# Optimization experiments

Measured on AMD Instinct MI355X. Metric: run time of the kernel, lower is better.

The kernel has to match this reference:

```python
import jax, jax.numpy as jnp
import numpy as np
from jax import lax

EPS = 1e-5

def _bn(x, p):
    # p: [4, C] = (gamma, beta, running_mean, running_var); x: [B,C,H,W] (eval-mode BN)
    g, b, m, v = p
    return (x - m[None, :, None, None]) * (g / jnp.sqrt(v + EPS))[None, :, None, None] + b[None, :, None, None]

def _relu6(x):
    return jnp.clip(x, 0.0, 6.0)

def _grouped_1x1(x, w):
    # x: [B, D, H, W], w: [G, D//G]; groups=G, 1 out channel per group (contiguous channel groups)
    B, D, H, W = x.shape
    G = w.shape[0]
    xr = x.reshape(B, G, D // G, H, W)
    return jnp.einsum('bgihw,gi->bghw', xr, w)

def _pool4(x, kind):
    if kind == 'max':
        return lax.reduce_window(x, -jnp.inf, lax.max, (1, 1, 4, 4), (1, 1, 4, 4), 'VALID')
    s = lax.reduce_window(x, 0.0, lax.add, (1, 1, 4, 4), (1, 1, 4, 4), 'VALID')
    return s / 16.0

def _rel_pos_index(rh):
    # Swin-style relative position index, static numpy
    coords = np.stack(np.meshgrid(np.arange(rh), np.arange(rh), indexing='ij')).reshape(2, -1)
    rel = coords[:, :, None] - coords[:, None, :]
    rel = rel.transpose(1, 2, 0).astype(np.int64)
    rel[..., 0] += rh - 1
    rel[..., 1] += rh - 1
    rel[..., 0] *= 2 * rh - 1
    return rel.sum(-1)  # [N, N]

def _upsample_bilinear_align(x, scale):
    # UpsamplingBilinear2d => align_corners=True
    B, C, H, W = x.shape
    Ho, Wo = H * scale, W * scale
    ys = jnp.linspace(0.0, H - 1.0, Ho)
    xs = jnp.linspace(0.0, W - 1.0, Wo)
    y0 = jnp.floor(ys).astype(jnp.int32); y1 = jnp.minimum(y0 + 1, H - 1); wy = (ys - y0)[None, None, :, None]
    x0 = jnp.floor(xs).astype(jnp.int32); x1 = jnp.minimum(x0 + 1, W - 1); wx = (xs - x0)[None, None, None, :]
    rows = x[:, :, y0, :] * (1.0 - wy) + x[:, :, y1, :] * wy          # [B,C,Ho,W]
    return rows[:, :, :, x0] * (1.0 - wx) + rows[:, :, :, x1] * wx    # [B,C,Ho,Wo]

def bh_attention(x, w_le, b_le, bn_le, w_max, b_max, bn_max, w_avg, b_avg, bn_avg,
                 bias_table, w_q, w_kv, w_proj, b_proj, w_out, b_out):
    D = x.shape[1]
    G = D // 4
    # q branch: 4x4 stride-4 grouped conv (groups=G, 4 in-ch per group) + BN + ReLU6
    xq = lax.conv_general_dilated(x, w_le, window_strides=(4, 4), padding='VALID',
                                  dimension_numbers=('NCHW', 'OIHW', 'NCHW'),
                                  feature_group_count=G)
    xq = _relu6(_bn(xq + b_le[None, :, None, None], bn_le))
    B, C, H, W = xq.shape
    N = H * W
    nH = 4 if C > 64 else 2
    hd = C // nH
    xq_t = xq.reshape(B, C, N).transpose(0, 2, 1)                      # [B,N,C]
    q = (xq_t @ w_q).reshape(B, N, nH, hd).transpose(0, 2, 1, 3) * (hd ** -0.5)

    def kv_branch(t, w_g, b_g, bn_g):
        t = _relu6(_bn(_grouped_1x1(t, w_g) + b_g[None, :, None, None], bn_g))
        tt = t.reshape(B, C, N).transpose(0, 2, 1)                     # [B,N,C]
        kv = (tt @ w_kv).reshape(B, N, 2, nH, hd).transpose(2, 0, 3, 1, 4)
        return kv[0], kv[1]                                            # [B,nH,N,hd]

    k1, v1 = kv_branch(_pool4(x, 'max'), w_max, b_max, bn_max)
    k2, v2 = kv_branch(_pool4(x, 'avg'), w_avg, b_avg, bn_avg)

    idx = _rel_pos_index(H)
    bias = bias_table[idx.reshape(-1)].reshape(N, N, nH).transpose(2, 0, 1)[None]  # [1,nH,N,N]

    def attend(k, v):
        attn = jax.nn.softmax(jnp.einsum('bhnd,bhmd->bhnm', q, k) + bias, axis=-1)
        o = jnp.einsum('bhnm,bhmd->bhnd', attn, v).transpose(0, 2, 1, 3).reshape(B, N, C)
        return o @ w_proj + b_proj

    x1 = attend(k1, v1).reshape(B, H, W, C).transpose(0, 3, 1, 2)
    x2 = attend(k2, v2).reshape(B, H, W, C).transpose(0, 3, 1, 2)
    out = x1 + x2
    out = jnp.einsum('bchw,oc->bohw', out, w_out) + b_out[None, :, None, None]
    return _upsample_bilinear_align(out, 4)


def setup_inputs() -> dict:
    key = jax.random.key(0)
    dim, h, B = 384, 128, 8
    C = dim // 4            # 96
    nH = 4 if C > 64 else 2
    rh = h // 4             # 32
    ks = jax.random.split(key, 12)
    bn_id = jnp.stack([jnp.ones(C), jnp.zeros(C), jnp.zeros(C), jnp.ones(C)])
    inp = {
        'x': jax.random.normal(ks[0], (B, dim, h, h), jnp.float32),
        'w_le': jax.random.normal(ks[1], (C, 4, 4, 4), jnp.float32) * 0.05,
        'b_le': jnp.zeros((C,), jnp.float32),
        'bn_le': bn_id,
        'w_max': jax.random.normal(ks[2], (C, 4), jnp.float32) * 0.1,
        'b_max': jnp.zeros((C,), jnp.float32),
        'bn_max': bn_id,
        'w_avg': jax.random.normal(ks[3], (C, 4), jnp.float32) * 0.1,
        'b_avg': jnp.zeros((C,), jnp.float32),
        'bn_avg': bn_id,
        'bias_table': jax.random.normal(ks[4], ((2 * rh - 1) ** 2, nH), jnp.float32) * 0.02,
        'w_q': jax.random.normal(ks[5], (C, C), jnp.float32) * (C ** -0.5),
        'w_kv': jax.random.normal(ks[6], (C, 2 * C), jnp.float32) * (C ** -0.5),
        'w_proj': jax.random.normal(ks[7], (C, C), jnp.float32) * (C ** -0.5),
        'b_proj': jnp.zeros((C,), jnp.float32),
        'w_out': jax.random.normal(ks[8], (dim, C), jnp.float32) * (C ** -0.5),
        'b_out': jnp.zeros((dim,), jnp.float32),
    }
    return inp


def reference(x, w_le, b_le, bn_le, w_max, b_max, bn_max, w_avg, b_avg, bn_avg,
              bias_table, w_q, w_kv, w_proj, b_proj, w_out, b_out):
    return bh_attention(x, w_le, b_le, bn_le, w_max, b_max, bn_max, w_avg, b_avg, bn_avg,
                        bias_table, w_q, w_kv, w_proj, b_proj, w_out, b_out)
```

## Files before the change

### kernel.cpp

```cpp
#include <hip/hip_runtime.h>
#include <math.h>

namespace {
constexpr int Bb  = 8;
constexpr int Dd  = 384;
constexpr int HIN = 128;
constexpr int Cc  = 96;
constexpr int Nn  = 1024;
constexpr int NH  = 4;
constexpr int HD  = 24;
}
#define BN_EPS 1e-5f
#define QSCALE 0.20412414523193154f

typedef unsigned short u16;
typedef unsigned int   u32;
typedef __attribute__((ext_vector_type(8))) short bh8;
typedef __attribute__((ext_vector_type(4))) float fx4;

#define MFMA16(a,b,c) __builtin_amdgcn_mfma_f32_16x16x32_bf16((a),(b),(c),0,0,0)

union PackU { u32 u[4]; bh8 s; };

__device__ __forceinline__ void split1(float v, u16& hi, u16& lo) {
    const u32 bv = __float_as_uint(v);
    const u32 hb = bv & 0xffff0000u;
    hi = (u16)(bv >> 16);
    const float r = v - __uint_as_float(hb);
    lo = (u16)(__float_as_uint(r) >> 16);
}
__device__ __forceinline__ void split2(float x, float y, u32& hi, u32& lo) {
    const u32 bx = __float_as_uint(x), by = __float_as_uint(y);
    const u32 hx = bx & 0xffff0000u, hy = by & 0xffff0000u;
    hi = (hx >> 16) | hy;
    const float rx = x - __uint_as_float(hx);
    const float ry = y - __uint_as_float(hy);
    lo = (__float_as_uint(rx) >> 16) | (__float_as_uint(ry) & 0xffff0000u);
}

__device__ __forceinline__ float bn_relu6(float y, const float* __restrict__ bn, int c) {
    float gam = bn[c], bet = bn[Cc + c], mu = bn[2*Cc + c], var = bn[3*Cc + c];
    float s = gam / sqrtf(var + BN_EPS);
    float r = (y - mu) * s + bet;
    return fminf(fmaxf(r, 0.0f), 6.0f);
}

__global__ __launch_bounds__(256) void stem_kernel(
    const float* __restrict__ x, const float* __restrict__ w_le,
    const float* __restrict__ b_le, const float* __restrict__ bn_le,
    const float* __restrict__ w_max, const float* __restrict__ b_max, const float* __restrict__ bn_max,
    const float* __restrict__ w_avg, const float* __restrict__ b_avg, const float* __restrict__ bn_avg,
    float* __restrict__ xq, float* __restrict__ tmx, float* __restrict__ tav)
{
    const int tid = threadIdx.x;
    const int n = blockIdx.x * 256 + tid;
    const int g = blockIdx.y;
    const int b = blockIdx.z;
    const int oh = n >> 5, ow = n & 31;

    const float* xb = x + (((size_t)b * Dd + 4*g) * HIN + 4*oh) * HIN + 4*ow;
    float conv = 0.0f, mxv = 0.0f, avv = 0.0f;
    #pragma unroll
    for (int i = 0; i < 4; ++i) {
        float cmax = -3.0e38f, csum = 0.0f;
        #pragma unroll
        for (int kh = 0; kh < 4; ++kh) {
            const float4 v = *(const float4*)(xb + ((size_t)i * HIN + kh) * HIN);
            const float* wl = w_le + (((g*4 + i)*4 + kh) * 4);
            conv = fmaf(v.x, wl[0], conv);
            conv = fmaf(v.y, wl[1], conv);
            conv = fmaf(v.z, wl[2], conv);
            conv = fmaf(v.w, wl[3], conv);
            cmax = fmaxf(cmax, fmaxf(fmaxf(v.x, v.y), fmaxf(v.z, v.w)));
            csum += (v.x + v.y) + (v.z + v.w);
        }
        mxv = fmaf(cmax, w_max[g*4 + i], mxv);
        avv = fmaf(csum * (1.0f/16.0f), w_avg[g*4 + i], avv);
    }
    const float xqv = bn_relu6(conv + b_le[g], bn_le, g);
    const float tm  = bn_relu6(mxv  + b_max[g], bn_max, g);
    const float ta  = bn_relu6(avv  + b_avg[g], bn_avg, g);
    const size_t o = ((size_t)b * Cc + g) * Nn + n;
    xq[o] = xqv; tmx[o] = tm; tav[o] = ta;
}

__global__ __launch_bounds__(256) void proj_kernel(
    const float* __restrict__ xq, const float* __restrict__ tmx, const float* __restrict__ tav,
    const float* __restrict__ w_q, const float* __restrict__ w_kv,
    u16* __restrict__ qhp, u16* __restrict__ qlp,
    u16* __restrict__ k1h, u16* __restrict__ k1l, u16* __restrict__ k2h, u16* __restrict__ k2l,
    u16* __restrict__ v1h, u16* __restrict__ v1l, u16* __restrict__ v2h, u16* __restrict__ v2l)
{
    const int tid = threadIdx.x;
    const int n0 = blockIdx.x * 32;
    const int b  = blockIdx.y;
    __shared__ float axq[32*101];
    __shared__ float amx[32*101];
    __shared__ float aav[32*101];
    __shared__ float lw[96*97];

    for (int e = tid; e < 96*32; e += 256) {
        const int c = e >> 5, j = e & 31;
        const size_t src = ((size_t)b * Cc + c) * Nn + n0 + j;
        axq[j*101 + c] = xq[src];
        amx[j*101 + c] = tmx[src];
        aav[j*101 + c] = tav[src];
    }

    const int tn = (tid & 7) * 4;
    const int tc = (tid >> 3) * 3;

    __syncthreads();
    for (int e = tid; e < 96*96; e += 256) lw[(e/96)*97 + (e%96)] = w_q[e];
    __syncthreads();
    {
        float acc[4][3] = {};
        for (int k = 0; k < 96; ++k) {
            const float w0 = lw[k*97 + tc + 0];
            const float w1 = lw[k*97 + tc + 1];
            const float w2 = lw[k*97 + tc + 2];
            #pragma unroll
            for (int i = 0; i < 4; ++i) {
                const float a = axq[(tn+i)*101 + k];
                acc[i][0] = fmaf(a, w0, acc[i][0]);
                acc[i][1] = fmaf(a, w1, acc[i][1]);
                acc[i][2] = fmaf(a, w2, acc[i][2]);
            }
        }
        #pragma unroll
        for (int j = 0; j < 3; ++j) {
            const int col = tc + j, hh = col / HD, d = col - hh*HD;
            #pragma unroll
            for (int i = 0; i < 4; ++i) {
                const int n = n0 + tn + i;
                u16 hi, lo;
                split1(acc[i][j] * QSCALE, hi, lo);
                const size_t dst = ((size_t)(b*NH + hh)*Nn + n)*32 + d;
                qhp[dst] = hi; qlp[dst] = lo;
            }
        }
    }

    __syncthreads();
    for (int e = tid; e < 96*96; e += 256) lw[(e/96)*97 + (e%96)] = w_kv[(e/96)*192 + (e%96)];
    __syncthreads();
    {
        float a1c[4][3] = {}, a2c[4][3] = {};
        for (int k = 0; k < 96; ++k) {
            const float w0 = lw[k*97 + tc + 0];
            const float w1 = lw[k*97 + tc + 1];
            const float w2 = lw[k*97 + tc + 2];
            #pragma unroll
            for (int i = 0; i < 4; ++i) {
                const float a1 = amx[(tn+i)*101 + k];
                const float a2 = aav[(tn+i)*101 + k];
                a1c[i][0] = fmaf(a1, w0, a1c[i][0]);
                a1c[i][1] = fmaf(a1, w1, a1c[i][1]);
                a1c[i][2] = fmaf(a1, w2, a1c[i][2]);
                a2c[i][0] = fmaf(a2, w0, a2c[i][0]);
                a2c[i][1] = fmaf(a2, w1, a2c[i][1]);
                a2c[i][2] = fmaf(a2, w2, a2c[i][2]);
            }
        }
        #pragma unroll
        for (int j = 0; j < 3; ++j) {
            const int col = tc + j, hh = col / HD, d = col - hh*HD;
            #pragma unroll
            for (int i = 0; i < 4; ++i) {
                const int n = n0 + tn + i;
                const int rho = (n & ~31) | ((n & 4) << 2) | ((n & 24) >> 1) | (n & 3);
                const size_t dst = ((size_t)(b*NH + hh)*Nn + rho)*32 + d;
                u16 hi, lo;
                split1(a1c[i][j], hi, lo); k1h[dst] = hi; k1l[dst] = lo;
                split1(a2c[i][j], hi, lo); k2h[dst] = hi; k2l[dst] = lo;
            }
        }
    }

    __syncthreads();
    for (int e = tid; e < 96*96; e += 256) lw[(e/96)*97 + (e%96)] = w_kv[(e/96)*192 + 96 + (e%96)];
    __syncthreads();
    {
        float a1c[4][3] = {}, a2c[4][3] = {};
        for (int k = 0; k < 96; ++k) {
            const float w0 = lw[k*97 + tc + 0];
            const float w1 = lw[k*97 + tc + 1];
            const float w2 = lw[k*97 + tc + 2];
            #pragma unroll
            for (int i = 0; i < 4; ++i) {
                const float a1 = amx[(tn+i)*101 + k];
                const float a2 = aav[(tn+i)*101 + k];
                a1c[i][0] = fmaf(a1, w0, a1c[i][0]);
                a1c[i][1] = fmaf(a1, w1, a1c[i][1]);
                a1c[i][2] = fmaf(a1, w2, a1c[i][2]);
                a2c[i][0] = fmaf(a2, w0, a2c[i][0]);
                a2c[i][1] = fmaf(a2, w1, a2c[i][1]);
                a2c[i][2] = fmaf(a2, w2, a2c[i][2]);
            }
        }
        #pragma unroll
        for (int j = 0; j < 3; ++j) {
            const int col = tc + j, hh = col / HD, d = col - hh*HD;
            #pragma unroll
            for (int i = 0; i < 4; ++i) {
                const int n = n0 + tn + i;
                const size_t dst = ((size_t)(b*NH + hh)*32 + d)*Nn + n;
                u16 hi, lo;
                split1(a1c[i][j], hi, lo); v1h[dst] = hi; v1l[dst] = lo;
                split1(a2c[i][j], hi, lo); v2h[dst] = hi; v2l[dst] = lo;
            }
        }
    }

    for (int e = tid; e < 1024; e += 256) {
        const int hh = e >> 8;
        const int nn = (e >> 3) & 31;
        const int d  = 24 + (e & 7);
        const int n  = n0 + nn;
        const size_t kd = ((size_t)(b*NH + hh)*Nn + n)*32 + d;
        qhp[kd] = 0; qlp[kd] = 0;
        k1h[kd] = 0; k1l[kd] = 0; k2h[kd] = 0; k2l[kd] = 0;
        const size_t vd = ((size_t)(b*NH + hh)*32 + d)*Nn + n;
        v1h[vd] = 0; v1l[vd] = 0; v2h[vd] = 0; v2l[vd] = 0;
    }
}

__global__ __launch_bounds__(256) void attn_kernel(
    const u16* __restrict__ qhp, const u16* __restrict__ qlp,
    const u16* __restrict__ k1h, const u16* __restrict__ k1l,
    const u16* __restrict__ k2h, const u16* __restrict__ k2l,
    const u16* __restrict__ v1h, const u16* __restrict__ v1l,
    const u16* __restrict__ v2h, const u16* __restrict__ v2l,
    const float* __restrict__ bias_table, float* __restrict__ osum)
{
    const int tid = threadIdx.x;
    const int h = blockIdx.y, b = blockIdx.z;
    const int bh = b*NH + h;

    __shared__ float biasl[3969];
    for (int e = tid; e < 3969; e += 256) biasl[e] = bias_table[e*NH + h];
    __syncthreads();

    const int lane = tid & 63;
    const int wave = tid >> 6;
    const int lg = lane >> 4;
    const int lr = lane & 15;
    const int q  = blockIdx.x*64 + wave*16 + lr;
    const int yn = q >> 5, xn = q & 31;

    const size_t qoff = ((size_t)bh*Nn + q)*32 + lg*8;
    const bh8 qfh = *(const bh8*)(qhp + qoff);
    const bh8 qfl = *(const bh8*)(qlp + qoff);

    const size_t kbase = ((size_t)bh*Nn + lr)*32 + lg*8;
    const u16* kp1h = k1h + kbase;
    const u16* kp1l = k1l + kbase;
    const u16* kp2h = k2h + kbase;
    const u16* kp2l = k2l + kbase;
    const size_t vbase = ((size_t)bh*32 + lr)*Nn + lg*8;
    const u16* vp1h = v1h + vbase;
    const u16* vp1l = v1l + vbase;
    const u16* vp2h = v2h + vbase;
    const u16* vp2l = v2l + vbase;

    const fx4 zero = {0.0f, 0.0f, 0.0f, 0.0f};
    fx4 o1[2], o2[2];
    o1[0] = zero; o1[1] = zero; o2[0] = zero; o2[1] = zero;
    float m1 = -3.0e38f, m2 = -3.0e38f, l1 = 0.0f, l2 = 0.0f;

    for (int it = 0; it < 16; ++it) {
        const int kb = it*64;
        fx4 s1[4], s2[4];
        #pragma unroll
        for (int t = 0; t < 4; ++t) {
            const int ro = (kb + t*16)*32;
            const bh8 a1h = *(const bh8*)(kp1h + ro);
            const bh8 a1l = *(const bh8*)(kp1l + ro);
            const bh8 a2h = *(const bh8*)(kp2h + ro);
            const bh8 a2l = *(const bh8*)(kp2l + ro);
            const int ym   = (kb >> 5) + (t >> 1);
            const int xmb  = (t & 1)*4 + lg*8;
            const int rowb = (yn - ym + 31)*63 + (xn + 31) - xmb;
            fx4 cb;
            #pragma unroll
            for (int j = 0; j < 4; ++j) cb[j] = biasl[rowb - j];
            fx4 u1 = cb, u2 = cb;
            u1 = MFMA16(a1h, qfh, u1);
            u1 = MFMA16(a1h, qfl, u1);
            u1 = MFMA16(a1l, qfh, u1);
            u2 = MFMA16(a2h, qfh, u2);
            u2 = MFMA16(a2h, qfl, u2);
            u2 = MFMA16(a2l, qfh, u2);
            s1[t] = u1; s2[t] = u2;
        }

        float t1 = s1[0][0], t2 = s2[0][0];
        #pragma unroll
        for (int t = 0; t < 4; ++t)
            #pragma unroll
            for (int j = 0; j < 4; ++j) {
                if (t | j) { t1 = fmaxf(t1, s1[t][j]); t2 = fmaxf(t2, s2[t][j]); }
            }
        t1 = fmaxf(t1, __shfl_xor(t1, 16));
        t1 = fmaxf(t1, __shfl_xor(t1, 32));
        t2 = fmaxf(t2, __shfl_xor(t2, 16));
        t2 = fmaxf(t2, __shfl_xor(t2, 32));
        const float M1 = fmaxf(m1, t1), M2 = fmaxf(m2, t2);
        const float c1 = __expf(m1 - M1), c2 = __expf(m2 - M2);
        m1 = M1; m2 = M2;
        l1 *= c1; l2 *= c2;
        o1[0] *= c1; o1[1] *= c1;
        o2[0] *= c2; o2[1] *= c2;

        float p1[4][4], p2[4][4];
        #pragma unroll
        for (int t = 0; t < 4; ++t)
            #pragma unroll
            for (int j = 0; j < 4; ++j) {
                const float e1 = __expf(s1[t][j] - M1);
                const float e2 = __expf(s2[t][j] - M2);
                p1[t][j] = e1; p2[t][j] = e2;
                l1 += e1; l2 += e2;
            }

        #pragma unroll
        for (int ch = 0; ch < 2; ++ch) {
            PackU b1h, b1l, b2h, b2l;
            split2(p1[2*ch  ][0], p1[2*ch  ][1], b1h.u[0], b1l.u[0]);
            split2(p1[2*ch  ][2], p1[2*ch  ][3], b1h.u[1], b1l.u[1]);
            split2(p1[2*ch+1][0], p1[2*ch+1][1], b1h.u[2], b1l.u[2]);
            split2(p1[2*ch+1][2], p1[2*ch+1][3], b1h.u[3], b1l.u[3]);
            split2(p2[2*ch  ][0], p2[2*ch  ][1], b2h.u[0], b2l.u[0]);
            split2(p2[2*ch  ][2], p2[2*ch  ][3], b2h.u[1], b2l.u[1]);
            split2(p2[2*ch+1][0], p2[2*ch+1][1], b2h.u[2], b2l.u[2]);
            split2(p2[2*ch+1][2], p2[2*ch+1][3], b2h.u[3], b2l.u[3]);
            const int vo0 = kb + ch*32;
            #pragma unroll
            for (int dt = 0; dt < 2; ++dt) {
                const size_t vo = (size_t)(dt*16)*Nn + vo0;
                const bh8 w1h = *(const bh8*)(vp1h + vo);
                const bh8 w1l = *(const bh8*)(vp1l + vo);
                const bh8 w2h = *(const bh8*)(vp2h + vo);
                const bh8 w2l = *(const bh8*)(vp2l + vo);
                o1[dt] = MFMA16(w1h, b1h.s, o1[dt]);
                o1[dt] = MFMA16(w1h, b1l.s, o1[dt]);
                o1[dt] = MFMA16(w1l, b1h.s, o1[dt]);
                o2[dt] = MFMA16(w2h, b2h.s, o2[dt]);
                o2[dt] = MFMA16(w2h, b2l.s, o2[dt]);
                o2[dt] = MFMA16(w2l, b2h.s, o2[dt]);
            }
        }
    }

    l1 += __shfl_xor(l1, 16); l1 += __shfl_xor(l1, 32);
    l2 += __shfl_xor(l2, 16); l2 += __shfl_xor(l2, 32);
    const float i1 = 1.0f / l1, i2 = 1.0f / l2;
    float* orow = osum + ((size_t)b*Nn + q)*Cc + h*HD;
    #pragma unroll
    for (int dt = 0; dt < 2; ++dt)
        #pragma unroll
        for (int j = 0; j < 4; ++j) {
            const int d = dt*16 + lg*4 + j;
            if (d < HD) orow[d] = o1[dt][j]*i1 + o2[dt][j]*i2;
        }
}

__global__ __launch_bounds__(256) void fusew_kernel(
    const float* __restrict__ w_proj, const float* __restrict__ b_proj,
    const float* __restrict__ w_out, const float* __restrict__ b_out,
    float* __restrict__ wf, float* __restrict__ bf)
{
    const int e = blockIdx.x * 256 + threadIdx.x;
    if (e < Cc * Dd) {
        const int c = e / Dd, o = e - c*Dd;
        const float* wp = w_proj + c*Cc;
        const float* wo = w_out + (size_t)o*Cc;
        float acc = 0.0f;
        for (int c2 = 0; c2 < Cc; ++c2) acc = fmaf(wp[c2], wo[c2], acc);
        wf[e] = acc;
    }
    if (e < Dd) {
        const float* wo = w_out + (size_t)e*Cc;
        float acc = 0.0f;
        for (int c = 0; c < Cc; ++c) acc = fmaf(b_proj[c], wo[c], acc);
        bf[e] = b_out[e] + 2.0f * acc;
    }
}

__global__ __launch_bounds__(256) void outgemm_kernel(
    const float* __restrict__ osum, const float* __restrict__ wf, const float* __restrict__ bf,
    float* __restrict__ outs)
{
    const int tid = threadIdx.x;
    const int n0 = blockIdx.x * 32;
    const int b  = blockIdx.y;
    __shared__ float ax[32*101];
    __shared__ float lw[96*132];
    for (int e = tid; e < 32*96; e += 256) {
        const int n = e / 96, c = e - n*96;
        ax[n*101 + c] = osum[((size_t)b*Nn + n0 + n)*Cc + c];
    }
    const int tn = (tid & 7) * 4;
    const int tj = (tid >> 3) * 4;
    for (int o0 = 0; o0 < Dd; o0 += 128) {
        __syncthreads();
        for (int e = tid; e < 96*128; e += 256) {
            const int c = e >> 7, j = e & 127;
            lw[c*132 + j] = wf[(size_t)c*Dd + o0 + j];
        }
        __syncthreads();
        float acc[4][4] = {};
        for (int c = 0; c < 96; ++c) {
            const float4 wv = *(const float4*)&lw[c*132 + tj];
            #pragma unroll
            for (int i = 0; i < 4; ++i) {
                const float a = ax[(tn+i)*101 + c];
                acc[i][0] = fmaf(a, wv.x, acc[i][0]);
                acc[i][1] = fmaf(a, wv.y, acc[i][1]);
                acc[i][2] = fmaf(a, wv.z, acc[i][2]);
                acc[i][3] = fmaf(a, wv.w, acc[i][3]);
            }
        }
        #pragma unroll
        for (int j = 0; j < 4; ++j) {
            const int o = o0 + tj + j;
            const float bb = bf[o];
            #pragma unroll
            for (int i = 0; i < 4; ++i)
                outs[((size_t)b*Dd + o)*Nn + n0 + tn + i] = acc[i][j] + bb;
        }
    }
}

__global__ __launch_bounds__(256) void upsample_kernel(
    const float* __restrict__ src, float* __restrict__ dst)
{
    const int gid = blockIdx.x * 256 + threadIdx.x;
    const int ox4 = gid & 31;
    const int oy  = (gid >> 5) & 127;
    const int bc  = gid >> 12;
    const float* s = src + (size_t)bc * 1024;
    const float sy = oy * (31.0f / 127.0f);
    const int y0 = (int)sy;
    const int y1 = min(y0 + 1, 31);
    const float wy = sy - (float)y0;
    const float* r0 = s + y0 * 32;
    const float* r1 = s + y1 * 32;
    float res[4];
    #pragma unroll
    for (int j = 0; j < 4; ++j) {
        const int ox = ox4 * 4 + j;
        const float sx = ox * (31.0f / 127.0f);
        const int x0 = (int)sx;
        const int x1 = min(x0 + 1, 31);
        const float wx = sx - (float)x0;
        const float t0 = r0[x0] * (1.0f - wx) + r0[x1] * wx;
        const float t1 = r1[x0] * (1.0f - wx) + r1[x1] * wx;
        res[j] = t0 * (1.0f - wy) + t1 * wy;
    }
    *(float4*)(dst + (size_t)gid * 4) = make_float4(res[0], res[1], res[2], res[3]);
}

extern "C" void kernel_launch(void* const* d_in, const int* in_sizes, int n_in,
                              void* d_out, int out_size, void* d_ws, size_t ws_size,
                              hipStream_t stream)
{
    const float* x      = (const float*)d_in[0];
    const float* w_le   = (const float*)d_in[1];
    const float* b_le   = (const float*)d_in[2];
    const float* bn_le  = (const float*)d_in[3];
    const float* w_max  = (const float*)d_in[4];
    const float* b_max  = (const float*)d_in[5];
    const float* bn_max = (const float*)d_in[6];
    const float* w_avg  = (const float*)d_in[7];
    const float* b_avg  = (const float*)d_in[8];
    const float* bn_avg = (const float*)d_in[9];
    const float* btab   = (const float*)d_in[10];
    const float* w_q    = (const float*)d_in[11];
    const float* w_kv   = (const float*)d_in[12];
    const float* w_proj = (const float*)d_in[13];
    const float* b_proj = (const float*)d_in[14];
    const float* w_out  = (const float*)d_in[15];
    const float* b_out  = (const float*)d_in[16];
    (void)in_sizes; (void)n_in; (void)out_size; (void)ws_size;

    float* ws = (float*)d_ws;
    const size_t T  = (size_t)Bb * Cc * Nn;
    const size_t AS = (size_t)Bb * NH * Nn * 32;

    float* xq   = ws + 0*T;
    float* tmx  = ws + 1*T;
    float* tav  = ws + 2*T;
    u16*  bb16  = (u16*)(ws + 3*T);
    u16* qh  = bb16 + 0*AS;  u16* ql  = bb16 + 1*AS;
    u16* k1h = bb16 + 2*AS;  u16* k1l = bb16 + 3*AS;
    u16* k2h = bb16 + 4*AS;  u16* k2l = bb16 + 5*AS;
    u16* v1h = bb16 + 6*AS;  u16* v1l = bb16 + 7*AS;
    u16* v2h = bb16 + 8*AS;  u16* v2l = bb16 + 9*AS;
    float* osum = (float*)(bb16 + 10*AS);
    float* wf   = osum + T;
    float* bf   = wf + (size_t)Cc*Dd;
    float* outs = ws;

    stem_kernel<<<dim3(4, 96, 8), 256, 0, stream>>>(
        x, w_le, b_le, bn_le, w_max, b_max, bn_max, w_avg, b_avg, bn_avg, xq, tmx, tav);
    proj_kernel<<<dim3(32, 8), 256, 0, stream>>>(
        xq, tmx, tav, w_q, w_kv, qh, ql, k1h, k1l, k2h, k2l, v1h, v1l, v2h, v2l);
    fusew_kernel<<<dim3(144), 256, 0, stream>>>(w_proj, b_proj, w_out, b_out, wf, bf);
    attn_kernel<<<dim3(16, 4, 8), 256, 0, stream>>>(
        qh, ql, k1h, k1l, k2h, k2l, v1h, v1l, v2h, v2l, btab, osum);
    outgemm_kernel<<<dim3(32, 8), 256, 0, stream>>>(osum, wf, bf, outs);
    upsample_kernel<<<dim3(49152), 256, 0, stream>>>(outs, (float*)d_out);
}
```

Measured before the change: 545.8 us.

## Split attention keys across waves with flash-decoding merge and serialize branches

The attention kernel now handles 32 queries per block instead of 64 and splits the 1024 keys between two wave pairs. Each pair runs its own online softmax, and the partial max, sum and output are merged through shared memory. The two softmax branches are processed one after the other rather than interleaved, which lowers register pressure, and a launch bound of 4 blocks per CU is set. The rescale is skipped when the running max does not change. Together these double the grid and raise occupancy on a kernel that was latency bound, at the cost of one barrier, a shared-memory merge step and the bias table being loaded twice as often.

```diff
diff --git a/kernel.cpp b/kernel.cpp
--- a/kernel.cpp
+++ b/kernel.cpp
@@ -225,7 +225,7 @@
     }
 }
 
-__global__ __launch_bounds__(256) void attn_kernel(
+__global__ __launch_bounds__(256, 4) void attn_kernel(
     const u16* __restrict__ qhp, const u16* __restrict__ qlp,
     const u16* __restrict__ k1h, const u16* __restrict__ k1l,
     const u16* __restrict__ k2h, const u16* __restrict__ k2l,
@@ -238,14 +238,18 @@
     const int bh = b*NH + h;
 
     __shared__ float biasl[3969];
+    __shared__ float mrg[2][64][21];
+
     for (int e = tid; e < 3969; e += 256) biasl[e] = bias_table[e*NH + h];
     __syncthreads();
 
     const int lane = tid & 63;
     const int wave = tid >> 6;
+    const int qg = wave & 1;
+    const int ks = wave >> 1;
     const int lg = lane >> 4;
     const int lr = lane & 15;
-    const int q  = blockIdx.x*64 + wave*16 + lr;
+    const int q  = blockIdx.x*32 + qg*16 + lr;
     const int yn = q >> 5, xn = q & 31;
 
     const size_t qoff = ((size_t)bh*Nn + q)*32 + lg*8;
@@ -253,116 +257,133 @@
     const bh8 qfl = *(const bh8*)(qlp + qoff);
 
     const size_t kbase = ((size_t)bh*Nn + lr)*32 + lg*8;
-    const u16* kp1h = k1h + kbase;
-    const u16* kp1l = k1l + kbase;
-    const u16* kp2h = k2h + kbase;
-    const u16* kp2l = k2l + kbase;
     const size_t vbase = ((size_t)bh*32 + lr)*Nn + lg*8;
-    const u16* vp1h = v1h + vbase;
-    const u16* vp1l = v1l + vbase;
-    const u16* vp2h = v2h + vbase;
-    const u16* vp2l = v2l + vbase;
+    const u16* kph[2] = { k1h + kbase, k2h + kbase };
+    const u16* kpl[2] = { k1l + kbase, k2l + kbase };
+    const u16* vph[2] = { v1h + vbase, v2h + vbase };
+    const u16* vpl[2] = { v1l + vbase, v2l + vbase };
 
     const fx4 zero = {0.0f, 0.0f, 0.0f, 0.0f};
-    fx4 o1[2], o2[2];
-    o1[0] = zero; o1[1] = zero; o2[0] = zero; o2[1] = zero;
-    float m1 = -3.0e38f, m2 = -3.0e38f, l1 = 0.0f, l2 = 0.0f;
-
-    for (int it = 0; it < 16; ++it) {
-        const int kb = it*64;
-        fx4 s1[4], s2[4];
-        #pragma unroll
-        for (int t = 0; t < 4; ++t) {
-            const int ro = (kb + t*16)*32;
-            const bh8 a1h = *(const bh8*)(kp1h + ro);
-            const bh8 a1l = *(const bh8*)(kp1l + ro);
-            const bh8 a2h = *(const bh8*)(kp2h + ro);
-            const bh8 a2l = *(const bh8*)(kp2l + ro);
-            const int ym   = (kb >> 5) + (t >> 1);
-            const int xmb  = (t & 1)*4 + lg*8;
-            const int rowb = (yn - ym + 31)*63 + (xn + 31) - xmb;
-            fx4 cb;
-            #pragma unroll
-            for (int j = 0; j < 4; ++j) cb[j] = biasl[rowb - j];
-            fx4 u1 = cb, u2 = cb;
-            u1 = MFMA16(a1h, qfh, u1);
-            u1 = MFMA16(a1h, qfl, u1);
-            u1 = MFMA16(a1l, qfh, u1);
-            u2 = MFMA16(a2h, qfh, u2);
-            u2 = MFMA16(a2h, qfl, u2);
-            u2 = MFMA16(a2l, qfh, u2);
-            s1[t] = u1; s2[t] = u2;
-        }
-
-        float t1 = s1[0][0], t2 = s2[0][0];
-        #pragma unroll
-        for (int t = 0; t < 4; ++t)
+    fx4 oo[2][2];
+    float mm[2], ll[2];
+
+    #pragma unroll
+    for (int br = 0; br < 2; ++br) {
+        oo[br][0] = zero; oo[br][1] = zero;
+        float m = -3.0e38f, l = 0.0f;
+        const u16* kh = kph[br]; const u16* kl = kpl[br];
+        const u16* vh = vph[br]; const u16* vl = vpl[br];
+
+        for (int it = ks*8; it < ks*8 + 8; ++it) {
+            const int kb = it*64;
+            fx4 s[4];
+            #pragma unroll
+            for (int t = 0; t < 4; ++t) {
+                const int ro = (kb + t*16)*32;
+                const bh8 ah = *(const bh8*)(kh + ro);
+                const bh8 al = *(const bh8*)(kl + ro);
+                const int ym   = (kb >> 5) + (t >> 1);
+                const int xmb  = (t & 1)*4 + lg*8;
+                const int rowb = (yn - ym + 31)*63 + (xn + 31) - xmb;
+                fx4 u;
+                #pragma unroll
+                for (int j = 0; j < 4; ++j) u[j] = biasl[rowb - j];
+                u = MFMA16(ah, qfh, u);
+                u = MFMA16(ah, qfl, u);
+                u = MFMA16(al, qfh, u);
+                s[t] = u;
+            }
+
+            float tmax = s[0][0];
+            #pragma unroll
+            for (int t = 0; t < 4; ++t)
+                #pragma unroll
+                for (int j = 0; j < 4; ++j)
+                    if (t | j) tmax = fmaxf(tmax, s[t][j]);
+            tmax = fmaxf(tmax, __shfl_xor(tmax, 16));
+            tmax = fmaxf(tmax, __shfl_xor(tmax, 32));
+            const float M = fmaxf(m, tmax);
+            if (!__all(tmax <= m)) {
+                const float c = __expf(m - M);
+                l *= c;
+                oo[br][0] *= c; oo[br][1] *= c;
+            }
+            m = M;
+
+            #pragma unroll
+            for (int ch = 0; ch < 2; ++ch) {
+                const float e0 = __expf(s[2*ch  ][0] - M);
+                const float e1 = __expf(s[2*ch  ][1] - M);
+                const float e2 = __expf(s[2*ch  ][2] - M);
+                const float e3 = __expf(s[2*ch  ][3] - M);
+                const float e4 = __expf(s[2*ch+1][0] - M);
+                const float e5 = __expf(s[2*ch+1][1] - M);
+                const float e6 = __expf(s[2*ch+1][2] - M);
+                const float e7 = __expf(s[2*ch+1][3] - M);
+                l += ((e0 + e1) + (e2 + e3)) + ((e4 + e5) + (e6 + e7));
+                PackU ph_, pl_;
+                split2(e0, e1, ph_.u[0], pl_.u[0]);
+                split2(e2, e3, ph_.u[1], pl_.u[1]);
+                split2(e4, e5, ph_.u[2], pl_.u[2]);
+                split2(e6, e7, ph_.u[3], pl_.u[3]);
+                const int vo0 = kb + ch*32;
+                #pragma unroll
+                for (int dt = 0; dt < 2; ++dt) {
+                    const size_t vo = (size_t)(dt*16)*Nn + vo0;
+                    const bh8 wh = *(const bh8*)(vh + vo);
+                    const bh8 wl = *(const bh8*)(vl + vo);
+                    oo[br][dt] = MFMA16(wh, ph_.s, oo[br][dt]);
+                    oo[br][dt] = MFMA16(wh, pl_.s, oo[br][dt]);
+                    oo[br][dt] = MFMA16(wl, ph_.s, oo[br][dt]);
+                }
+            }
+        }
+        mm[br] = m; ll[br] = l;
+    }
+
+    if (ks == 1) {
+        float* mb = &mrg[qg][lane][0];
+        #pragma unroll
+        for (int br = 0; br < 2; ++br) {
+            mb[br*10 + 0] = mm[br];
+            mb[br*10 + 1] = ll[br];
             #pragma unroll
             for (int j = 0; j < 4; ++j) {
-                if (t | j) { t1 = fmaxf(t1, s1[t][j]); t2 = fmaxf(t2, s2[t][j]); }
-            }
-        t1 = fmaxf(t1, __shfl_xor(t1, 16));
-        t1 = fmaxf(t1, __shfl_xor(t1, 32));
-        t2 = fmaxf(t2, __shfl_xor(t2, 16));
-        t2 = fmaxf(t2, __shfl_xor(t2, 32));
-        const float M1 = fmaxf(m1, t1), M2 = fmaxf(m2, t2);
-        const float c1 = __expf(m1 - M1), c2 = __expf(m2 - M2);
-        m1 = M1; m2 = M2;
-        l1 *= c1; l2 *= c2;
-        o1[0] *= c1; o1[1] *= c1;
-        o2[0] *= c2; o2[1] *= c2;
-
-        float p1[4][4], p2[4][4];
-        #pragma unroll
-        for (int t = 0; t < 4; ++t)
+                mb[br*10 + 2 + j] = oo[br][0][j];
+                mb[br*10 + 6 + j] = oo[br][1][j];
+            }
+        }
+    }
+    __syncthreads();
+    if (ks == 0) {
+        const float* mb = &mrg[qg][lane][0];
+        float li[2]; fx4 om[2][2];
+        #pragma unroll
+        for (int br = 0; br < 2; ++br) {
+            const float mo  = mb[br*10 + 0];
+            const float lo2 = mb[br*10 + 1];
+            const float M  = fmaxf(mm[br], mo);
+            const float ca = __expf(mm[br] - M);
+            const float cb = __expf(mo - M);
+            float lm = ll[br]*ca + lo2*cb;
+            #pragma unroll
+            for (int dt = 0; dt < 2; ++dt)
+                #pragma unroll
+                for (int j = 0; j < 4; ++j)
+                    om[br][dt][j] = oo[br][dt][j]*ca + mb[br*10 + 2 + dt*4 + j]*cb;
+            lm += __shfl_xor(lm, 16);
+            lm += __shfl_xor(lm, 32);
+            li[br] = 1.0f / lm;
+        }
+        float* orow = osum + ((size_t)b*Nn + q)*Cc + h*HD;
+        #pragma unroll
+        for (int dt = 0; dt < 2; ++dt)
             #pragma unroll
             for (int j = 0; j < 4; ++j) {
-                const float e1 = __expf(s1[t][j] - M1);
-                const float e2 = __expf(s2[t][j] - M2);
-                p1[t][j] = e1; p2[t][j] = e2;
-                l1 += e1; l2 += e2;
-            }
-
-        #pragma unroll
-        for (int ch = 0; ch < 2; ++ch) {
-            PackU b1h, b1l, b2h, b2l;
-            split2(p1[2*ch  ][0], p1[2*ch  ][1], b1h.u[0], b1l.u[0]);
-            split2(p1[2*ch  ][2], p1[2*ch  ][3], b1h.u[1], b1l.u[1]);
-            split2(p1[2*ch+1][0], p1[2*ch+1][1], b1h.u[2], b1l.u[2]);
-            split2(p1[2*ch+1][2], p1[2*ch+1][3], b1h.u[3], b1l.u[3]);
-            split2(p2[2*ch  ][0], p2[2*ch  ][1], b2h.u[0], b2l.u[0]);
-            split2(p2[2*ch  ][2], p2[2*ch  ][3], b2h.u[1], b2l.u[1]);
-            split2(p2[2*ch+1][0], p2[2*ch+1][1], b2h.u[2], b2l.u[2]);
-            split2(p2[2*ch+1][2], p2[2*ch+1][3], b2h.u[3], b2l.u[3]);
-            const int vo0 = kb + ch*32;
-            #pragma unroll
-            for (int dt = 0; dt < 2; ++dt) {
-                const size_t vo = (size_t)(dt*16)*Nn + vo0;
-                const bh8 w1h = *(const bh8*)(vp1h + vo);
-                const bh8 w1l = *(const bh8*)(vp1l + vo);
-                const bh8 w2h = *(const bh8*)(vp2h + vo);
-                const bh8 w2l = *(const bh8*)(vp2l + vo);
-                o1[dt] = MFMA16(w1h, b1h.s, o1[dt]);
-                o1[dt] = MFMA16(w1h, b1l.s, o1[dt]);
-                o1[dt] = MFMA16(w1l, b1h.s, o1[dt]);
-                o2[dt] = MFMA16(w2h, b2h.s, o2[dt]);
-                o2[dt] = MFMA16(w2h, b2l.s, o2[dt]);
-                o2[dt] = MFMA16(w2l, b2h.s, o2[dt]);
-            }
-        }
-    }
-
-    l1 += __shfl_xor(l1, 16); l1 += __shfl_xor(l1, 32);
-    l2 += __shfl_xor(l2, 16); l2 += __shfl_xor(l2, 32);
-    const float i1 = 1.0f / l1, i2 = 1.0f / l2;
-    float* orow = osum + ((size_t)b*Nn + q)*Cc + h*HD;
-    #pragma unroll
-    for (int dt = 0; dt < 2; ++dt)
-        #pragma unroll
-        for (int j = 0; j < 4; ++j) {
-            const int d = dt*16 + lg*4 + j;
-            if (d < HD) orow[d] = o1[dt][j]*i1 + o2[dt][j]*i2;
-        }
+                const int d = dt*16 + lg*4 + j;
+                if (d < HD) orow[d] = om[0][dt][j]*li[0] + om[1][dt][j]*li[1];
+            }
+    }
 }
 
 __global__ __launch_bounds__(256) void fusew_kernel(
@@ -507,7 +528,7 @@
     proj_kernel<<<dim3(32, 8), 256, 0, stream>>>(
         xq, tmx, tav, w_q, w_kv, qh, ql, k1h, k1l, k2h, k2l, v1h, v1l, v2h, v2l);
     fusew_kernel<<<dim3(144), 256, 0, stream>>>(w_proj, b_proj, w_out, b_out, wf, bf);
-    attn_kernel<<<dim3(16, 4, 8), 256, 0, stream>>>(
+    attn_kernel<<<dim3(32, 4, 8), 256, 0, stream>>>(
         qh, ql, k1h, k1l, k2h, k2l, v1h, v1l, v2h, v2l, btab, osum);
     outgemm_kernel<<<dim3(32, 8), 256, 0, stream>>>(osum, wf, bf, outs);
     upsample_kernel<<<dim3(49152), 256, 0, stream>>>(outs, (float*)d_out);
```

Measured after the change: 546.0 us. No clear change (+0.0%).
